# Kernel tuning notes

Hardware: AMD Instinct MI355X
Metric: run time of the kernel (lower is better)

Reference implementation:

```python
import jax, jax.numpy as jnp
import numpy as np

NEG = -1e9  # masked_fill value


def _forward(input1, input2, wg1, wg2):
    S, E = input1.shape[0], wg1.shape[0]
    k = E // 4                      # expert_group_size
    num_2nd = E // 4
    capacity = int(2 * ((S + num_2nd - 1) // num_2nd))  # training-mode capacity, cf=1.0

    # --- first-level group gating ---
    group_logits = input1 @ wg1.T                     # [S,E]
    group_gates = jax.nn.softmax(group_logits.at[:, 0].set(NEG), axis=1)
    _, top_idx = jax.lax.top_k(group_gates, k)        # [S,k]
    rows = jnp.arange(S)[:, None]
    group_mask = jnp.zeros((S, E), dtype=bool).at[rows, top_idx].set(True)

    # --- second-level logits, masked to the selected group ---
    logits = input2 @ wg2.T                           # [S,E]
    gates = jax.nn.softmax(jnp.where(group_mask, logits, NEG), axis=1)

    # --- htop1gating ---
    indices1 = jnp.argmax(gates, axis=1)              # [S]
    mask1 = jax.nn.one_hot(indices1, E, dtype=jnp.int32)   # [S,E]
    gates1_s = (gates * mask1).sum(axis=1)            # [S]
    locations1 = jnp.cumsum(mask1, axis=0) - 1        # [S,E]

    me = jnp.mean(gates, axis=0)
    ce = jnp.mean(mask1.astype(gates.dtype), axis=0)
    l_aux = jnp.sum(me * ce) / num_2nd * (E * E)

    mask1 = mask1 * (locations1 < capacity).astype(mask1.dtype)
    locations1_s = jnp.sum(locations1 * mask1, axis=1)          # [S]
    gates1 = gates1_s[:, None] * mask1.astype(gates1_s.dtype)   # [S,E]
    locations1_sc = jax.nn.one_hot(locations1_s, capacity, dtype=gates1.dtype)  # [S,C]
    combine = gates1[:, :, None] * locations1_sc[:, None, :]    # [S,E,C]
    dispatch = combine.astype(bool)
    return l_aux, combine, dispatch


def setup_inputs() -> dict:
    key = jax.random.key(0)
    k1, k2, k3, k4 = jax.random.split(key, 4)
    S, D, E = 4096, 1024, 64
    return {
        "input1": jax.random.normal(k1, (S, D), dtype=jnp.float32),
        "input2": jax.random.normal(k2, (S, D), dtype=jnp.float32),
        "wg1": jax.random.normal(k3, (E, D), dtype=jnp.float32) * 0.02,
        "wg2": jax.random.normal(k4, (E, D), dtype=jnp.float32) * 0.02,
    }


def reference(input1, input2, wg1, wg2):
    return _forward(input1, input2, wg1, wg2)
```

## Files before the change

### kernel.cpp

```cpp
#include <hip/hip_runtime.h>
#include <cstdint>
#include <cstddef>

#define S_ROWS 4096
#define DIM 1024
#define NE 64
#define CAP 512
#define NEGV -1e9f
#define NGEMM 128
#define NFILL 4096

typedef float v4f __attribute__((ext_vector_type(4)));

__global__ __launch_bounds__(256) void fusedA(const float* __restrict__ X1, const float* __restrict__ W1,
                                              const float* __restrict__ X2, const float* __restrict__ W2,
                                              int* __restrict__ eidx, float* __restrict__ gval,
                                              float* __restrict__ Gslot, int* __restrict__ Cslot,
                                              v4f* __restrict__ out4, long long n4,
                                              float* __restrict__ out, long long n) {
    const int bid = blockIdx.x;
    const int tid = threadIdx.x;

    __shared__ float As[32][68];
    __shared__ float Bs[64][68];
    __shared__ float Lg[2][32][68];
    __shared__ float sG[4][NE];
    __shared__ int   hist[NE];

    if (bid >= NGEMM) {
        long long i = (long long)(bid - NGEMM) * 256 + tid;
        const long long stride = (long long)(gridDim.x - NGEMM) * 256;
        v4f z = {0.f, 0.f, 0.f, 0.f};
        for (; i < n4; i += stride) __builtin_nontemporal_store(z, &out4[i]);
        if (bid == NGEMM && tid == 0)
            for (long long j = n4 * 4; j < n; ++j) out[j] = 0.f;
        return;
    }

    if (tid < NE) hist[tid] = 0;

    const int row0 = bid * 32;
    const int tx = tid & 15;
    const int ty = tid >> 4;

    #pragma unroll
    for (int m = 0; m < 2; ++m) {
        const float* __restrict__ X = m ? X2 : X1;
        const float* __restrict__ W = m ? W2 : W1;
        float acc[2][4] = {};
        for (int kk = 0; kk < DIM; kk += 64) {
            __syncthreads();
            #pragma unroll
            for (int p = 0; p < 2; ++p) {
                int r  = ty + p * 16;
                int c4 = tx * 4;
                float4 a = *(const float4*)&X[(size_t)(row0 + r) * DIM + kk + c4];
                *(float4*)&As[r][c4] = a;
            }
            #pragma unroll
            for (int p = 0; p < 4; ++p) {
                int e  = ty + p * 16;
                int c4 = tx * 4;
                float4 w = *(const float4*)&W[(size_t)e * DIM + kk + c4];
                Bs[c4 + 0][e] = w.x;
                Bs[c4 + 1][e] = w.y;
                Bs[c4 + 2][e] = w.z;
                Bs[c4 + 3][e] = w.w;
            }
            __syncthreads();
            #pragma unroll
            for (int k4 = 0; k4 < 64; k4 += 4) {
                float4 a[2], b[4];
                #pragma unroll
                for (int i = 0; i < 2; ++i) a[i] = *(float4*)&As[ty * 2 + i][k4];
                #pragma unroll
                for (int t = 0; t < 4; ++t) b[t] = *(float4*)&Bs[k4 + t][tx * 4];
                #pragma unroll
                for (int i = 0; i < 2; ++i) {
                    acc[i][0] += a[i].x * b[0].x + a[i].y * b[1].x + a[i].z * b[2].x + a[i].w * b[3].x;
                    acc[i][1] += a[i].x * b[0].y + a[i].y * b[1].y + a[i].z * b[2].y + a[i].w * b[3].y;
                    acc[i][2] += a[i].x * b[0].z + a[i].y * b[1].z + a[i].z * b[2].z + a[i].w * b[3].z;
                    acc[i][3] += a[i].x * b[0].w + a[i].y * b[1].w + a[i].z * b[2].w + a[i].w * b[3].w;
                }
            }
        }
        #pragma unroll
        for (int i = 0; i < 2; ++i)
            #pragma unroll
            for (int t = 0; t < 4; ++t)
                Lg[m][ty * 2 + i][tx * 4 + t] = acc[i][t];
    }
    __syncthreads();

    const int wid = tid >> 6, lane = tid & 63;
    float gacc = 0.f;
    #pragma unroll
    for (int i = 0; i < 8; ++i) {
        const int lr = wid * 8 + i;
        const int r  = row0 + lr;
        float l1 = Lg[0][lr][lane];
        if (lane == 0) l1 = NEGV;

        int cnt = 0;
        #pragma unroll
        for (int j = 0; j < 64; ++j) {
            float vj = __shfl(l1, j);
            cnt += (vj > l1 || (vj == l1 && j < lane));
        }
        const bool sel = cnt < 16;

        float l2 = Lg[1][lr][lane];
        float ml = sel ? l2 : NEGV;

        float mx = ml;
        #pragma unroll
        for (int o = 32; o; o >>= 1) mx = fmaxf(mx, __shfl_xor(mx, o));
        float ex = expf(ml - mx);
        float sum = ex;
        #pragma unroll
        for (int o = 32; o; o >>= 1) sum += __shfl_xor(sum, o);
        float g = ex / sum;
        gacc += g;

        float bg = g; int bi = lane;
        #pragma unroll
        for (int o = 32; o; o >>= 1) {
            float og = __shfl_xor(bg, o);
            int   oi = __shfl_xor(bi, o);
            if (og > bg || (og == bg && oi < bi)) { bg = og; bi = oi; }
        }
        if (lane == 0) {
            eidx[r] = bi;
            gval[r] = bg;
            atomicAdd(&hist[bi], 1);
        }
    }
    sG[wid][lane] = gacc;
    __syncthreads();
    if (tid < NE) {
        Gslot[bid * NE + tid] = sG[0][tid] + sG[1][tid] + sG[2][tid] + sG[3][tid];
        Cslot[bid * NE + tid] = hist[tid];
    }
}

__global__ __launch_bounds__(256) void finishB(const int* __restrict__ eidx, const float* __restrict__ gval,
                                               const float* __restrict__ Gslot, const int* __restrict__ Cslot,
                                               float* __restrict__ out) {
    const int s = blockIdx.x;
    if (s == S_ROWS) {
        if (threadIdx.x < NE) {
            const int e = threadIdx.x;
            float Ge = 0.f; int Ce = 0;
            for (int b = 0; b < NGEMM; ++b) {
                Ge += Gslot[b * NE + e];
                Ce += Cslot[b * NE + e];
            }
            float v = Ge * (float)Ce;
            #pragma unroll
            for (int o = 32; o; o >>= 1) v += __shfl_xor(v, o);
            if (e == 0) out[0] = v * (1.0f / 65536.0f);
        }
        return;
    }
    const int my = eidx[s];
    int cnt = 0;
    for (int j = threadIdx.x; j < s; j += 256) cnt += (eidx[j] == my);
    __shared__ int sc[4];
    #pragma unroll
    for (int o = 32; o; o >>= 1) cnt += __shfl_down(cnt, o);
    const int wid = threadIdx.x >> 6, lane = threadIdx.x & 63;
    if (lane == 0) sc[wid] = cnt;
    __syncthreads();
    if (threadIdx.x == 0) {
        int rank = sc[0] + sc[1] + sc[2] + sc[3];
        if (rank < CAP) {
            size_t base = 1 + (((size_t)s * NE + my) * CAP + (size_t)rank);
            out[base] = gval[s];
            out[base + (size_t)S_ROWS * NE * CAP] = 1.0f;
        }
    }
}

extern "C" void kernel_launch(void* const* d_in, const int* in_sizes, int n_in,
                              void* d_out, int out_size, void* d_ws, size_t ws_size,
                              hipStream_t stream) {
    const float* in1 = (const float*)d_in[0];
    const float* in2 = (const float*)d_in[1];
    const float* wg1 = (const float*)d_in[2];
    const float* wg2 = (const float*)d_in[3];
    float* out = (float*)d_out;

    int*   eidx  = (int*)d_ws;
    float* gv    = (float*)(eidx + S_ROWS);
    float* Gslot = gv + S_ROWS;
    int*   Cslot = (int*)(Gslot + NGEMM * NE);

    long long n  = (long long)out_size;
    long long n4 = n >> 2;

    fusedA<<<NGEMM + NFILL, 256, 0, stream>>>(in1, wg1, in2, wg2,
                                              eidx, gv, Gslot, Cslot,
                                              (v4f*)out, n4, out, n);
    finishB<<<S_ROWS + 1, 256, 0, stream>>>(eidx, gv, Gslot, Cslot, out);
}
```

Baseline: 1.071 ms.

## Compute slot ranks first, then write output in one dense pass

The separate zero-fill pass and the scattered writes of nonzero entries are replaced by a single streaming fill. In that fill each float4 works out from a compact per-row slot code whether it holds a gate value or a dispatch flag. Ranks are now found from per-block histograms plus a short local scan in a small kernel, instead of one block per row scanning all earlier rows. This removes a second scattered write pass and the quadratic rank scan. In exchange there is an extra kernel launch and serialisation: the fill can no longer overlap with the GEMM, and it does a small index lookup per vector.

```diff
diff --git a/kernel.cpp b/kernel.cpp
--- a/kernel.cpp
+++ b/kernel.cpp
@@ -12,12 +12,10 @@
 
 typedef float v4f __attribute__((ext_vector_type(4)));
 
-__global__ __launch_bounds__(256) void fusedA(const float* __restrict__ X1, const float* __restrict__ W1,
-                                              const float* __restrict__ X2, const float* __restrict__ W2,
-                                              int* __restrict__ eidx, float* __restrict__ gval,
-                                              float* __restrict__ Gslot, int* __restrict__ Cslot,
-                                              v4f* __restrict__ out4, long long n4,
-                                              float* __restrict__ out, long long n) {
+__global__ __launch_bounds__(256) void gateA(const float* __restrict__ X1, const float* __restrict__ W1,
+                                             const float* __restrict__ X2, const float* __restrict__ W2,
+                                             int* __restrict__ eidx, float* __restrict__ gval,
+                                             float* __restrict__ Gslot, int* __restrict__ Cslot) {
     const int bid = blockIdx.x;
     const int tid = threadIdx.x;
 
@@ -26,16 +24,6 @@
     __shared__ float Lg[2][32][68];
     __shared__ float sG[4][NE];
     __shared__ int   hist[NE];
-
-    if (bid >= NGEMM) {
-        long long i = (long long)(bid - NGEMM) * 256 + tid;
-        const long long stride = (long long)(gridDim.x - NGEMM) * 256;
-        v4f z = {0.f, 0.f, 0.f, 0.f};
-        for (; i < n4; i += stride) __builtin_nontemporal_store(z, &out4[i]);
-        if (bid == NGEMM && tid == 0)
-            for (long long j = n4 * 4; j < n; ++j) out[j] = 0.f;
-        return;
-    }
 
     if (tid < NE) hist[tid] = 0;
 
@@ -143,13 +131,15 @@
     }
 }
 
-__global__ __launch_bounds__(256) void finishB(const int* __restrict__ eidx, const float* __restrict__ gval,
-                                               const float* __restrict__ Gslot, const int* __restrict__ Cslot,
-                                               float* __restrict__ out) {
-    const int s = blockIdx.x;
-    if (s == S_ROWS) {
-        if (threadIdx.x < NE) {
-            const int e = threadIdx.x;
+__global__ __launch_bounds__(256) void rankB(const int* __restrict__ eidx,
+                                             const float* __restrict__ Gslot, const int* __restrict__ Cslot,
+                                             unsigned int* __restrict__ hrow, float* __restrict__ laux) {
+    const int bid = blockIdx.x;
+    const int tid = threadIdx.x;
+
+    if (bid == 16) {
+        if (tid < NE) {
+            const int e = tid;
             float Ge = 0.f; int Ce = 0;
             for (int b = 0; b < NGEMM; ++b) {
                 Ge += Gslot[b * NE + e];
@@ -158,26 +148,80 @@
             float v = Ge * (float)Ce;
             #pragma unroll
             for (int o = 32; o; o >>= 1) v += __shfl_xor(v, o);
-            if (e == 0) out[0] = v * (1.0f / 65536.0f);
+            if (e == 0) laux[0] = v * (1.0f / 65536.0f);
         }
         return;
     }
-    const int my = eidx[s];
-    int cnt = 0;
-    for (int j = threadIdx.x; j < s; j += 256) cnt += (eidx[j] == my);
-    __shared__ int sc[4];
-    #pragma unroll
-    for (int o = 32; o; o >>= 1) cnt += __shfl_down(cnt, o);
-    const int wid = threadIdx.x >> 6, lane = threadIdx.x & 63;
-    if (lane == 0) sc[wid] = cnt;
+
+    __shared__ int Cs[NGEMM * NE];
+    __shared__ int Es[256];
+    for (int t = tid; t < NGEMM * NE; t += 256) Cs[t] = Cslot[t];
+    const int s = bid * 256 + tid;
+    Es[tid] = eidx[s];
     __syncthreads();
-    if (threadIdx.x == 0) {
-        int rank = sc[0] + sc[1] + sc[2] + sc[3];
-        if (rank < CAP) {
-            size_t base = 1 + (((size_t)s * NE + my) * CAP + (size_t)rank);
-            out[base] = gval[s];
-            out[base + (size_t)S_ROWS * NE * CAP] = 1.0f;
-        }
+
+    const int e  = Es[tid];
+    const int b0 = s >> 5;
+    int rank = 0;
+    for (int b = 0; b < b0; ++b) rank += Cs[b * NE + e];
+    for (int jl = (tid & ~31); jl < tid; ++jl) rank += (Es[jl] == e);
+
+    hrow[s] = (rank < CAP) ? ((unsigned int)(e << 9) | (unsigned int)rank)
+                           : 0xFFFFFFFFu;
+}
+
+__global__ __launch_bounds__(256) void fillC(const unsigned int* __restrict__ hrow,
+                                             const float* __restrict__ gval,
+                                             const float* __restrict__ laux,
+                                             v4f* __restrict__ out4, long long n4,
+                                             float* __restrict__ out, long long n) {
+    const unsigned int M27 = (1u << 27) - 1u;
+    long long i = (long long)blockIdx.x * 256 + threadIdx.x;
+    const long long stride = (long long)gridDim.x * 256;
+
+    if (i == 0) {
+        v4f z = {laux[0], 0.f, 0.f, 0.f};
+        unsigned int h = hrow[0];
+        if (h <= 2u) {
+            float g0 = gval[0];
+            if (h == 0u) z.y = g0; else if (h == 1u) z.z = g0; else z.w = g0;
+        }
+        __builtin_nontemporal_store(z, &out4[0]);
+        for (long long f = 4 * n4; f < n; ++f) {
+            unsigned int p = (unsigned int)(f - 1);
+            unsigned int t = p >> 27, s = (p & M27) >> 15;
+            unsigned int h2 = hrow[s];
+            float v = 0.f;
+            if (((t << 27) | (s << 15) | h2) == p) v = t ? 1.0f : gval[s];
+            out[f] = v;
+        }
+        i += stride;
+    }
+
+    for (; i < n4; i += stride) {
+        unsigned int p0 = (unsigned int)(4 * i) - 1u;
+        unsigned int t0 = p0 >> 27;
+        unsigned int s0 = (p0 & M27) >> 15;
+        unsigned int h0 = hrow[s0];
+        unsigned int j0 = ((t0 << 27) | (s0 << 15) | h0) - p0;
+
+        unsigned int p3 = p0 + 3u;
+        unsigned int t1 = p3 >> 27;
+        unsigned int s1 = (p3 & M27) >> 15;
+        unsigned int h1 = h0;
+        if (s1 != s0) h1 = hrow[s1];
+        unsigned int j1 = ((t1 << 27) | (s1 << 15) | h1) - p0;
+
+        v4f z = {0.f, 0.f, 0.f, 0.f};
+        if (j0 <= 3u || j1 <= 3u) {
+            float va = t0 ? 1.0f : gval[s0];
+            float vb = t1 ? 1.0f : gval[s1];
+            float e0 = 0.f, e1 = 0.f, e2 = 0.f, e3 = 0.f;
+            if (j0 == 0u) e0 = va; if (j0 == 1u) e1 = va; if (j0 == 2u) e2 = va; if (j0 == 3u) e3 = va;
+            if (j1 == 0u) e0 = vb; if (j1 == 1u) e1 = vb; if (j1 == 2u) e2 = vb; if (j1 == 3u) e3 = vb;
+            z.x = e0; z.y = e1; z.z = e2; z.w = e3;
+        }
+        __builtin_nontemporal_store(z, &out4[i]);
     }
 }
 
@@ -190,16 +234,17 @@
     const float* wg2 = (const float*)d_in[3];
     float* out = (float*)d_out;
 
-    int*   eidx  = (int*)d_ws;
-    float* gv    = (float*)(eidx + S_ROWS);
-    float* Gslot = gv + S_ROWS;
-    int*   Cslot = (int*)(Gslot + NGEMM * NE);
+    int*          eidx  = (int*)d_ws;
+    float*        gv    = (float*)(eidx + S_ROWS);
+    float*        Gslot = gv + S_ROWS;
+    int*          Cslot = (int*)(Gslot + NGEMM * NE);
+    unsigned int* hrow  = (unsigned int*)(Cslot + NGEMM * NE);
+    float*        laux  = (float*)(hrow + S_ROWS);
 
     long long n  = (long long)out_size;
     long long n4 = n >> 2;
 
-    fusedA<<<NGEMM + NFILL, 256, 0, stream>>>(in1, wg1, in2, wg2,
-                                              eidx, gv, Gslot, Cslot,
-                                              (v4f*)out, n4, out, n);
-    finishB<<<S_ROWS + 1, 256, 0, stream>>>(eidx, gv, Gslot, Cslot, out);
-}
+    gateA<<<NGEMM, 256, 0, stream>>>(in1, wg1, in2, wg2, eidx, gv, Gslot, Cslot);
+    rankB<<<17, 256, 0, stream>>>(eidx, Gslot, Cslot, hrow, laux);
+    fillC<<<NFILL, 256, 0, stream>>>(hrow, gv, laux, (v4f*)out, n4, out, n);
+}
```

Measured after the change: 1.204 ms. 1.12x slower.

## Compute capacity ranks from per-block histograms instead of O(S^2) scans

Applied to the files above, without the earlier changes.

The finish kernel now computes each token's position within its expert as a prefix sum over the per-GEMM-block expert histograms plus a local count inside its 32-row block. It launches 17 blocks instead of one block per token doing a linear scan over all earlier tokens. The zero-fill also switches from nontemporal stores to ordinary stores. This removes quadratic work and thousands of block launches, at the cost of a 32KB shared-memory histogram copy per block and a serial loop of up to 128 iterations per thread.

```diff
diff --git a/kernel.cpp b/kernel.cpp
--- a/kernel.cpp
+++ b/kernel.cpp
@@ -31,7 +31,7 @@
         long long i = (long long)(bid - NGEMM) * 256 + tid;
         const long long stride = (long long)(gridDim.x - NGEMM) * 256;
         v4f z = {0.f, 0.f, 0.f, 0.f};
-        for (; i < n4; i += stride) __builtin_nontemporal_store(z, &out4[i]);
+        for (; i < n4; i += stride) out4[i] = z;
         if (bid == NGEMM && tid == 0)
             for (long long j = n4 * 4; j < n; ++j) out[j] = 0.f;
         return;
@@ -143,13 +143,15 @@
     }
 }
 
-__global__ __launch_bounds__(256) void finishB(const int* __restrict__ eidx, const float* __restrict__ gval,
+__global__ __launch_bounds__(256) void finishC(const int* __restrict__ eidx, const float* __restrict__ gval,
                                                const float* __restrict__ Gslot, const int* __restrict__ Cslot,
                                                float* __restrict__ out) {
-    const int s = blockIdx.x;
-    if (s == S_ROWS) {
-        if (threadIdx.x < NE) {
-            const int e = threadIdx.x;
+    const int bid = blockIdx.x;
+    const int tid = threadIdx.x;
+
+    if (bid == 16) {
+        if (tid < NE) {
+            const int e = tid;
             float Ge = 0.f; int Ce = 0;
             for (int b = 0; b < NGEMM; ++b) {
                 Ge += Gslot[b * NE + e];
@@ -162,22 +164,24 @@
         }
         return;
     }
-    const int my = eidx[s];
-    int cnt = 0;
-    for (int j = threadIdx.x; j < s; j += 256) cnt += (eidx[j] == my);
-    __shared__ int sc[4];
-    #pragma unroll
-    for (int o = 32; o; o >>= 1) cnt += __shfl_down(cnt, o);
-    const int wid = threadIdx.x >> 6, lane = threadIdx.x & 63;
-    if (lane == 0) sc[wid] = cnt;
+
+    __shared__ int Cs[NGEMM * NE];
+    __shared__ int Es[256];
+    for (int t = tid; t < NGEMM * NE; t += 256) Cs[t] = Cslot[t];
+    const int s = bid * 256 + tid;
+    Es[tid] = eidx[s];
     __syncthreads();
-    if (threadIdx.x == 0) {
-        int rank = sc[0] + sc[1] + sc[2] + sc[3];
-        if (rank < CAP) {
-            size_t base = 1 + (((size_t)s * NE + my) * CAP + (size_t)rank);
-            out[base] = gval[s];
-            out[base + (size_t)S_ROWS * NE * CAP] = 1.0f;
-        }
+
+    const int e  = Es[tid];
+    const int b0 = s >> 5;
+    int rank = 0;
+    for (int b = 0; b < b0; ++b) rank += Cs[b * NE + e];
+    for (int jl = (tid & ~31); jl < tid; ++jl) rank += (Es[jl] == e);
+
+    if (rank < CAP) {
+        size_t base = 1 + (((size_t)s * NE + e) * CAP + (size_t)rank);
+        out[base] = gval[s];
+        out[base + (size_t)S_ROWS * NE * CAP] = 1.0f;
     }
 }
 
@@ -201,5 +205,5 @@
     fusedA<<<NGEMM + NFILL, 256, 0, stream>>>(in1, wg1, in2, wg2,
                                               eidx, gv, Gslot, Cslot,
                                               (v4f*)out, n4, out, n);
-    finishB<<<S_ROWS + 1, 256, 0, stream>>>(eidx, gv, Gslot, Cslot, out);
+    finishC<<<17, 256, 0, stream>>>(eidx, gv, Gslot, Cslot, out);
 }
```

Result: slower. 1.096 ms (+2.4%).
